# Kernel tuning notes

Hardware: AMD Instinct MI355X
Metric: run time of the kernel (lower is better)

The kernel has to match this reference:

```python
import jax, jax.numpy as jnp
import numpy as np
from jax import lax

IN_CH = 256
NF = 128
B, H, W = 8, 256, 256


def _bn_relu(y, s, b):
    # inference-mode BatchNorm folded into per-channel affine, then ReLU
    return jax.nn.relu(y * s[None, :, None, None] + b[None, :, None, None])


def _upsample_bilinear_ac(x, scale):
    # bilinear upsample, align_corners=True (matches torch nn.Upsample)
    b, c, h, w = x.shape
    Ho, Wo = h * scale, w * scale
    ys = jnp.arange(Ho, dtype=x.dtype) * ((h - 1) / (Ho - 1))
    xs = jnp.arange(Wo, dtype=x.dtype) * ((w - 1) / (Wo - 1))
    y0 = jnp.floor(ys).astype(jnp.int32)
    x0 = jnp.floor(xs).astype(jnp.int32)
    y1 = jnp.minimum(y0 + 1, h - 1)
    x1 = jnp.minimum(x0 + 1, w - 1)
    wy = (ys - y0.astype(x.dtype))[None, None, :, None]
    wx = (xs - x0.astype(x.dtype))[None, None, None, :]
    # interpolate rows then columns
    top = x[:, :, y0, :] * (1 - wy) + x[:, :, y1, :] * wy      # [b,c,Ho,w]
    out = top[:, :, :, x0] * (1 - wx) + top[:, :, :, x1] * wx  # [b,c,Ho,Wo]
    return out


def setup_inputs() -> dict:
    key = jax.random.key(0)
    ks = jax.random.split(key, 6)
    inp = {
        "x": jax.random.normal(ks[0], (B, 64, H, W), dtype=jnp.float32),
        "w1": jax.random.normal(ks[1], (IN_CH, 64, 8, 8), dtype=jnp.float32) * 0.02,
        "bn1_s": jnp.ones((IN_CH,), jnp.float32),
        "bn1_b": jnp.zeros((IN_CH,), jnp.float32),
        "w_fai": jax.random.normal(ks[2], (NF, IN_CH), dtype=jnp.float32) * 0.05,
        "bnf_s": jnp.ones((NF,), jnp.float32),
        "bnf_b": jnp.zeros((NF,), jnp.float32),
        "w_sit": jax.random.normal(ks[3], (NF, IN_CH), dtype=jnp.float32) * 0.05,
        "bns_s": jnp.ones((NF,), jnp.float32),
        "bns_b": jnp.zeros((NF,), jnp.float32),
        "w_gama": jax.random.normal(ks[4], (NF, IN_CH), dtype=jnp.float32) * 0.05,
        "bng_s": jnp.ones((NF,), jnp.float32),
        "bng_b": jnp.zeros((NF,), jnp.float32),
    }
    return inp


def reference(x, w1, bn1_s, bn1_b, w_fai, bnf_s, bnf_b, w_sit, bns_s, bns_b,
              w_gama, bng_s, bng_b):
    # conv1: 8x8 stride-8 conv, BN, ReLU  -> [B, IN_CH, h, w]
    y = lax.conv_general_dilated(x, w1, window_strides=(8, 8), padding="VALID",
                                 dimension_numbers=("NCHW", "OIHW", "NCHW"))
    y = _bn_relu(y, bn1_s, bn1_b)
    b, c, h, w = y.shape
    n = h * w
    # 1x1 conv projections (einsum), BN, ReLU
    fai = _bn_relu(jnp.einsum("bchw,oc->bohw", y, w_fai), bnf_s, bnf_b)
    sit = _bn_relu(jnp.einsum("bchw,oc->bohw", y, w_sit), bns_s, bns_b)
    gama = _bn_relu(jnp.einsum("bchw,oc->bohw", y, w_gama), bng_s, bng_b)
    fai = fai.reshape(b, NF, n)
    sit = sit.reshape(b, NF, n)
    gama = gama.reshape(b, NF, n)
    # non-local attention: sigmoid(fai^T sit) @ gama^T
    sf = jax.nn.sigmoid(jnp.einsum("bcn,bcm->bnm", fai, sit))  # [b, n, n]
    out = jnp.einsum("bnm,bcm->bcn", sf, gama)                  # [b, NF, n]
    out = out.reshape(b, NF, h, w)
    return _upsample_bilinear_ac(out, 8)
```

## Files before the change

kernel.cpp:

```cpp
#include <hip/hip_runtime.h>

typedef __attribute__((ext_vector_type(8))) short short8_t;
typedef __attribute__((ext_vector_type(4))) float float4_t;

__device__ __forceinline__ unsigned short f2bf(float f) {
    unsigned int u = __float_as_uint(f);
    return (unsigned short)((u + 0x7FFFu + ((u >> 16) & 1u)) >> 16);
}
__device__ __forceinline__ unsigned int pkbf(float a, float b) {
    return (unsigned int)f2bf(a) | ((unsigned int)f2bf(b) << 16);
}

__global__ __launch_bounds__(256) void k_wprep(
    const float* __restrict__ w1, unsigned short* __restrict__ w1s)
{
    const int id = blockIdx.x * 256 + threadIdx.x;
    const float4* s = (const float4*)(w1 + id * 8);
    float4 a = s[0], b = s[1];
    int4 o;
    o.x = pkbf(a.x, a.y); o.y = pkbf(a.z, a.w);
    o.z = pkbf(b.x, b.y); o.w = pkbf(b.z, b.w);
    *(int4*)(w1s + id * 8) = o;
}

__global__ __launch_bounds__(256, 2) void k_conv1(
    const float* __restrict__ x, const unsigned short* __restrict__ w1s,
    float* __restrict__ part)
{
    __shared__ unsigned short At[64 * 40];
    __shared__ unsigned short Bt[256 * 40];
    const int tid = threadIdx.x;
    const int mt = blockIdx.x, kc = blockIdx.y;
    const int m0 = mt * 64;
    const int bi = mt >> 4;
    const int oh0 = (mt & 15) * 2;
    const int lane = tid & 63, wid = tid >> 6;
    const int wn = wid;
    const int quad = lane >> 4, r16 = lane & 15;
    const int ow  = tid & 31;
    const int khl = (tid >> 5) & 3;
    const int ohl = tid >> 7;
    const int rowA  = ohl * 32 + ow;
    const int koffA = (khl ^ ((rowA >> 1) & 3)) * 8;
    const int kbase = kc * 1024;
    float4_t acc[4][4] = {};
    float4 ra0, ra1;
    int4 rb[4];

    {
        const int k0 = kbase;
        const int ic = k0 >> 6, kh0 = (k0 >> 3) & 7;
        const int xr = (oh0 + ohl) * 8 + kh0 + khl;
        const float4* s4 = (const float4*)(x + (((bi * 64 + ic) * 256 + xr) * 256 + ow * 8));
        ra0 = s4[0]; ra1 = s4[1];
        #pragma unroll
        for (int l = 0; l < 4; ++l) {
            const int slot = l * 256 + tid;
            const int row = slot >> 2, p = slot & 3;
            rb[l] = *(const int4*)(w1s + row * 4096 + k0 + p * 8);
        }
    }
    for (int it = 0; it < 32; ++it) {
        {
            int4 pa;
            pa.x = pkbf(ra0.x, ra0.y); pa.y = pkbf(ra0.z, ra0.w);
            pa.z = pkbf(ra1.x, ra1.y); pa.w = pkbf(ra1.z, ra1.w);
            *(int4*)&At[rowA * 40 + koffA] = pa;
            #pragma unroll
            for (int l = 0; l < 4; ++l) {
                const int slot = l * 256 + tid;
                const int row = slot >> 2, p = slot & 3;
                *(int4*)&Bt[row * 40 + p * 8] = rb[l];
            }
        }
        __syncthreads();
        if (it + 1 < 32) {
            const int k0 = kbase + (it + 1) * 32;
            const int ic = k0 >> 6, kh0 = (k0 >> 3) & 7;
            const int xr = (oh0 + ohl) * 8 + kh0 + khl;
            const float4* s4 = (const float4*)(x + (((bi * 64 + ic) * 256 + xr) * 256 + ow * 8));
            ra0 = s4[0]; ra1 = s4[1];
            #pragma unroll
            for (int l = 0; l < 4; ++l) {
                const int slot = l * 256 + tid;
                const int row = slot >> 2, p = slot & 3;
                rb[l] = *(const int4*)(w1s + row * 4096 + k0 + p * 8);
            }
        }
        short8_t aF[4], bF[4];
        #pragma unroll
        for (int i = 0; i < 4; ++i) {
            const int R = i * 16 + r16;
            aF[i] = *(const short8_t*)&At[R * 40 + (quad ^ ((r16 >> 1) & 3)) * 8];
        }
        #pragma unroll
        for (int j = 0; j < 4; ++j)
            bF[j] = *(const short8_t*)&Bt[(wn * 64 + j * 16 + r16) * 40 + quad * 8];
        #pragma unroll
        for (int i = 0; i < 4; ++i)
            #pragma unroll
            for (int j = 0; j < 4; ++j)
                acc[i][j] = __builtin_amdgcn_mfma_f32_16x16x32_bf16(aF[i], bF[j], acc[i][j], 0, 0, 0);
        __syncthreads();
    }
    float* pp = part + ((size_t)kc << 21);
    #pragma unroll
    for (int i = 0; i < 4; ++i) {
        const int mg = m0 + i * 16 + quad * 4;
        #pragma unroll
        for (int j = 0; j < 4; ++j) {
            const int ng = wn * 64 + j * 16 + r16;
            #pragma unroll
            for (int r = 0; r < 4; ++r)
                pp[(mg + r) * 256 + ng] = acc[i][j][r];
        }
    }
}

__global__ __launch_bounds__(256, 4) void k_reduce(
    const float* __restrict__ part, const float* __restrict__ s1,
    const float* __restrict__ b1, unsigned short* __restrict__ y)
{
    const int id = blockIdx.x * 256 + threadIdx.x;
    const int c4 = id & 63;
    const float4* p = (const float4*)part + id;
    float4 a = p[0], b = p[524288], c = p[1048576], d = p[1572864];
    float4 s = ((const float4*)s1)[c4], bb = ((const float4*)b1)[c4];
    float vx = fmaxf((a.x + b.x + c.x + d.x) * s.x + bb.x, 0.f);
    float vy = fmaxf((a.y + b.y + c.y + d.y) * s.y + bb.y, 0.f);
    float vz = fmaxf((a.z + b.z + c.z + d.z) * s.z + bb.z, 0.f);
    float vw = fmaxf((a.w + b.w + c.w + d.w) * s.w + bb.w, 0.f);
    int2 o; o.x = pkbf(vx, vy); o.y = pkbf(vz, vw);
    ((int2*)y)[id] = o;
}

__global__ __launch_bounds__(256, 2) void k_proj3(
    const unsigned short* __restrict__ y,
    const float* __restrict__ w_fai, const float* __restrict__ w_sit,
    const float* __restrict__ w_gama,
    const float* __restrict__ fs, const float* __restrict__ fb,
    const float* __restrict__ ss, const float* __restrict__ sb,
    const float* __restrict__ gs, const float* __restrict__ gb,
    unsigned short* __restrict__ P, unsigned short* __restrict__ G)
{
    __shared__ unsigned short At[64 * 40];
    __shared__ unsigned short Bt[64 * 40];
    const int tid = threadIdx.x;
    const int nt = blockIdx.x, mt = blockIdx.y;
    const int m0 = mt * 64;
    const float *W, *S, *Bb;
    if (nt < 2)      { W = w_fai;  S = fs; Bb = fb; }
    else if (nt < 4) { W = w_sit;  S = ss; Bb = sb; }
    else             { W = w_gama; S = gs; Bb = gb; }
    const int roff = (nt * 64) & 127;
    const int lane = tid & 63, wid = tid >> 6;
    const int wm = wid & 1, wn = wid >> 1;
    const int quad = lane >> 4, r16 = lane & 15;
    float4_t acc[2][2] = {};

    for (int k0 = 0; k0 < 256; k0 += 32) {
        {
            const int row = tid >> 2, pp = tid & 3;
            *(int4*)&At[row * 40 + pp * 8] =
                *(const int4*)(y + (m0 + row) * 256 + k0 + pp * 8);
        }
        #pragma unroll
        for (int l = 0; l < 2; ++l) {
            const int slot = l * 256 + tid;
            const int row = slot >> 3, pp = slot & 7;
            float4 v = *(const float4*)(W + (roff + row) * 256 + k0 + pp * 4);
            int2 wv; wv.x = pkbf(v.x, v.y); wv.y = pkbf(v.z, v.w);
            *(int2*)&Bt[row * 40 + pp * 4] = wv;
        }
        __syncthreads();
        short8_t aF[2], bF[2];
        #pragma unroll
        for (int i = 0; i < 2; ++i)
            aF[i] = *(const short8_t*)&At[(wm * 32 + i * 16 + r16) * 40 + quad * 8];
        #pragma unroll
        for (int j = 0; j < 2; ++j)
            bF[j] = *(const short8_t*)&Bt[(wn * 32 + j * 16 + r16) * 40 + quad * 8];
        #pragma unroll
        for (int i = 0; i < 2; ++i)
            #pragma unroll
            for (int j = 0; j < 2; ++j)
                acc[i][j] = __builtin_amdgcn_mfma_f32_16x16x32_bf16(aF[i], bF[j], acc[i][j], 0, 0, 0);
        __syncthreads();
    }
    #pragma unroll
    for (int i = 0; i < 2; ++i) {
        const int mg = m0 + wm * 32 + i * 16 + quad * 4;
        #pragma unroll
        for (int j = 0; j < 2; ++j) {
            const int nl = wn * 32 + j * 16 + r16;
            const float sc = S[roff + nl], bc = Bb[roff + nl];
            if (nt < 4) {
                const int col = nt * 64 + nl;
                #pragma unroll
                for (int r = 0; r < 4; ++r) {
                    float v = fmaxf(acc[i][j][r] * sc + bc, 0.f);
                    P[(mg + r) * 256 + col] = f2bf(v);
                }
            } else {
                const int c = roff + nl;
                #pragma unroll
                for (int r = 0; r < 4; ++r) {
                    float v = fmaxf(acc[i][j][r] * sc + bc, 0.f);
                    const int sp = mg + r;
                    G[((sp >> 10) * 128 + c) * 1024 + (sp & 1023)] = f2bf(v);
                }
            }
        }
    }
}

#define LSTR 152
__global__ __launch_bounds__(256, 2) void k_attn(
    const unsigned short* __restrict__ P, const unsigned short* __restrict__ G,
    float* __restrict__ Opart)
{
    __shared__ unsigned short At[64 * LSTR];
    __shared__ unsigned short Bt[128 * LSTR];
    __shared__ unsigned short Sl[64 * LSTR];
    const int tid = threadIdx.x;
    const int nt = blockIdx.x, zz = blockIdx.y;
    const int b = zz >> 2, kc = zz & 3;
    const int n0 = nt * 64;
    const int base = b * 1024;
    const int lane = tid & 63, wid = tid >> 6;
    const int wm = wid & 1, wn = wid >> 1;
    const int quad = lane >> 4, r16 = lane & 15;
    float4_t acc2[2][4] = {};

    #pragma unroll
    for (int l = 0; l < 4; ++l) {
        const int slot = l * 256 + tid;
        const int row = slot >> 4, p = slot & 15;
        *(int4*)&At[row * LSTR + p * 8] =
            *(const int4*)(P + (base + n0 + row) * 256 + p * 8);
    }
    for (int ms = 0; ms < 2; ++ms) {
        const int m1 = kc * 256 + ms * 128;
        #pragma unroll
        for (int l = 0; l < 8; ++l) {
            const int slot = l * 256 + tid;
            const int row = slot >> 4, p = slot & 15;
            *(int4*)&Bt[row * LSTR + p * 8] =
                *(const int4*)(P + (base + m1 + row) * 256 + 128 + p * 8);
        }
        __syncthreads();
        float4_t acc1[2][4] = {};
        #pragma unroll
        for (int c = 0; c < 4; ++c) {
            short8_t aF[2], bF[4];
            #pragma unroll
            for (int i = 0; i < 2; ++i)
                aF[i] = *(const short8_t*)&At[(wm * 32 + i * 16 + r16) * LSTR + c * 32 + quad * 8];
            #pragma unroll
            for (int j = 0; j < 4; ++j)
                bF[j] = *(const short8_t*)&Bt[(wn * 64 + j * 16 + r16) * LSTR + c * 32 + quad * 8];
            #pragma unroll
            for (int i = 0; i < 2; ++i)
                #pragma unroll
                for (int j = 0; j < 4; ++j)
                    acc1[i][j] = __builtin_amdgcn_mfma_f32_16x16x32_bf16(aF[i], bF[j], acc1[i][j], 0, 0, 0);
        }
        __syncthreads();
        #pragma unroll
        for (int i = 0; i < 2; ++i) {
            const int nl = wm * 32 + i * 16 + quad * 4;
            #pragma unroll
            for (int j = 0; j < 4; ++j) {
                const int ml = wn * 64 + j * 16 + r16;
                #pragma unroll
                for (int r = 0; r < 4; ++r) {
                    const float xv = acc1[i][j][r];
                    const float e = __expf(-xv);
                    const float v = __builtin_amdgcn_rcpf(1.0f + e);
                    Sl[(nl + r) * LSTR + ml] = f2bf(v);
                }
            }
        }
        #pragma unroll
        for (int l = 0; l < 8; ++l) {
            const int slot = l * 256 + tid;
            const int row = slot >> 4, p = slot & 15;
            *(int4*)&Bt[row * LSTR + p * 8] =
                *(const int4*)(G + (b * 128 + row) * 1024 + m1 + p * 8);
        }
        __syncthreads();
        #pragma unroll
        for (int c = 0; c < 4; ++c) {
            short8_t aF[2], bF[4];
            #pragma unroll
            for (int i = 0; i < 2; ++i)
                aF[i] = *(const short8_t*)&Sl[(wm * 32 + i * 16 + r16) * LSTR + c * 32 + quad * 8];
            #pragma unroll
            for (int j = 0; j < 4; ++j)
                bF[j] = *(const short8_t*)&Bt[(wn * 64 + j * 16 + r16) * LSTR + c * 32 + quad * 8];
            #pragma unroll
            for (int i = 0; i < 2; ++i)
                #pragma unroll
                for (int j = 0; j < 4; ++j)
                    acc2[i][j] = __builtin_amdgcn_mfma_f32_16x16x32_bf16(aF[i], bF[j], acc2[i][j], 0, 0, 0);
        }
        __syncthreads();
    }
    float* op = Opart + (size_t)kc * 1048576 + (size_t)b * 131072;
    #pragma unroll
    for (int i = 0; i < 2; ++i) {
        const int nl = n0 + wm * 32 + i * 16 + quad * 4;
        #pragma unroll
        for (int j = 0; j < 4; ++j) {
            const int ch = wn * 64 + j * 16 + r16;
            #pragma unroll
            for (int r = 0; r < 4; ++r)
                op[(nl + r) * 128 + ch] = acc2[i][j][r];
        }
    }
}

__global__ __launch_bounds__(256, 2) void k_up(
    const float* __restrict__ Opart, float* __restrict__ out)
{
    __shared__ float l0[32 * 136];
    __shared__ float l1[32 * 136];
    const int tid = threadIdx.x;
    const int yb = blockIdx.x, b = blockIdx.y;
    const float sc = 31.0f / 255.0f;
    const float fy = yb * sc;
    const int y0 = (int)fy;
    const float wy = fy - (float)y0;
    const int y1 = (y0 + 1 < 32) ? y0 + 1 : 31;
    const float4* r0 = (const float4*)(Opart + (size_t)b * 131072 + y0 * 4096);
    const float4* r1 = (const float4*)(Opart + (size_t)b * 131072 + y1 * 4096);
    #pragma unroll
    for (int j = 0; j < 4; ++j) {
        const int id = j * 256 + tid;
        const int xs = id >> 5, c4 = id & 31;
        float4 a0 = r0[id], a1 = r1[id];
        #pragma unroll
        for (int kc = 1; kc < 4; ++kc) {
            float4 t0 = r0[id + kc * 262144], t1 = r1[id + kc * 262144];
            a0.x += t0.x; a0.y += t0.y; a0.z += t0.z; a0.w += t0.w;
            a1.x += t1.x; a1.y += t1.y; a1.z += t1.z; a1.w += t1.w;
        }
        *(float4*)(l0 + xs * 136 + c4 * 4) = a0;
        *(float4*)(l1 + xs * 136 + c4 * 4) = a1;
    }
    __syncthreads();
    const float fx = tid * sc;
    const int x0 = (int)fx;
    const float wx = fx - (float)x0;
    const int x1 = (x0 + 1 < 32) ? x0 + 1 : 31;
    const float w00 = (1.f - wy) * (1.f - wx), w01 = (1.f - wy) * wx;
    const float w10 = wy * (1.f - wx), w11 = wy * wx;
    const float* a = l0 + x0 * 136;
    const float* bq = l0 + x1 * 136;
    const float* c = l1 + x0 * 136;
    const float* d = l1 + x1 * 136;
    float* op = out + (size_t)b * 8388608 + yb * 256 + tid;
    #pragma unroll 4
    for (int ch = 0; ch < 128; ++ch)
        op[ch * 65536] = w00 * a[ch] + w01 * bq[ch] + w10 * c[ch] + w11 * d[ch];
}

extern "C" void kernel_launch(void* const* d_in, const int* in_sizes, int n_in,
                              void* d_out, int out_size, void* d_ws, size_t ws_size,
                              hipStream_t stream) {
    (void)in_sizes; (void)n_in; (void)out_size; (void)ws_size;
    const float* x      = (const float*)d_in[0];
    const float* w1     = (const float*)d_in[1];
    const float* bn1_s  = (const float*)d_in[2];
    const float* bn1_b  = (const float*)d_in[3];
    const float* w_fai  = (const float*)d_in[4];
    const float* bnf_s  = (const float*)d_in[5];
    const float* bnf_b  = (const float*)d_in[6];
    const float* w_sit  = (const float*)d_in[7];
    const float* bns_s  = (const float*)d_in[8];
    const float* bns_b  = (const float*)d_in[9];
    const float* w_gama = (const float*)d_in[10];
    const float* bng_s  = (const float*)d_in[11];
    const float* bng_b  = (const float*)d_in[12];
    float* out = (float*)d_out;

    char* ws = (char*)d_ws;
    float*          pc    = (float*)ws;
    float*          Opart = (float*)(ws + 16u * 1024 * 1024);
    unsigned short* y     = (unsigned short*)(ws + 32u * 1024 * 1024);
    unsigned short* P     = (unsigned short*)(ws + 36u * 1024 * 1024);
    unsigned short* G     = (unsigned short*)(ws + 40u * 1024 * 1024);
    unsigned short* w1s   = (unsigned short*)(ws + 44u * 1024 * 1024);

    k_wprep <<<dim3(512),      256, 0, stream>>>(w1, w1s);
    k_conv1 <<<dim3(128, 4),   256, 0, stream>>>(x, w1s, pc);
    k_reduce<<<dim3(2048),     256, 0, stream>>>(pc, bn1_s, bn1_b, y);
    k_proj3 <<<dim3(6, 128),   256, 0, stream>>>(y, w_fai, w_sit, w_gama,
                                                 bnf_s, bnf_b, bns_s, bns_b,
                                                 bng_s, bng_b, P, G);
    k_attn  <<<dim3(16, 32),   256, 0, stream>>>(P, G, Opart);
    k_up    <<<dim3(256, 8),   256, 0, stream>>>(Opart, out);
}
```

Baseline: 510.1 us.

## Enlarge conv1 M-tile to 128 with 8 warps and split load roles

```diff
diff --git a/kernel.cpp b/kernel.cpp
--- a/kernel.cpp
+++ b/kernel.cpp
@@ -23,52 +23,58 @@
     *(int4*)(w1s + id * 8) = o;
 }
 
-__global__ __launch_bounds__(256, 2) void k_conv1(
+__global__ __launch_bounds__(512, 2) void k_conv1(
     const float* __restrict__ x, const unsigned short* __restrict__ w1s,
     float* __restrict__ part)
 {
-    __shared__ unsigned short At[64 * 40];
+    __shared__ unsigned short At[128 * 40];
     __shared__ unsigned short Bt[256 * 40];
     const int tid = threadIdx.x;
     const int mt = blockIdx.x, kc = blockIdx.y;
-    const int m0 = mt * 64;
-    const int bi = mt >> 4;
-    const int oh0 = (mt & 15) * 2;
+    const int m0 = mt * 128;
+    const int bi = mt >> 3;
+    const int oh0 = (mt & 7) * 4;
     const int lane = tid & 63, wid = tid >> 6;
-    const int wn = wid;
+    const int wm = wid & 1, wn = wid >> 1;
     const int quad = lane >> 4, r16 = lane & 15;
-    const int ow  = tid & 31;
-    const int khl = (tid >> 5) & 3;
-    const int ohl = tid >> 7;
-    const int rowA  = ohl * 32 + ow;
-    const int koffA = (khl ^ ((rowA >> 1) & 3)) * 8;
+    const bool isA = tid < 256;
+    const int tA = tid & 255;
+    const int rA = tA >> 4, segA = tA & 15;
+    const int ohl = rA >> 2, khl = rA & 3;
+    const int rowA = ohl * 32 + segA * 2;
+    const int koffA = (khl ^ (segA & 3)) * 8;
     const int kbase = kc * 1024;
     float4_t acc[4][4] = {};
-    float4 ra0, ra1;
+    float4 ra[4];
     int4 rb[4];
 
-    {
-        const int k0 = kbase;
-        const int ic = k0 >> 6, kh0 = (k0 >> 3) & 7;
+    if (isA) {
+        const int ic = kbase >> 6, kh0 = (kbase >> 3) & 7;
         const int xr = (oh0 + ohl) * 8 + kh0 + khl;
-        const float4* s4 = (const float4*)(x + (((bi * 64 + ic) * 256 + xr) * 256 + ow * 8));
-        ra0 = s4[0]; ra1 = s4[1];
+        const float4* s4 = (const float4*)(x + (((bi * 64 + ic) * 256 + xr) * 256 + segA * 16));
+        ra[0] = s4[0]; ra[1] = s4[1]; ra[2] = s4[2]; ra[3] = s4[3];
+    } else {
         #pragma unroll
         for (int l = 0; l < 4; ++l) {
-            const int slot = l * 256 + tid;
+            const int slot = l * 256 + tA;
             const int row = slot >> 2, p = slot & 3;
-            rb[l] = *(const int4*)(w1s + row * 4096 + k0 + p * 8);
-        }
-    }
+            rb[l] = *(const int4*)(w1s + row * 4096 + kbase + p * 8);
+        }
+    }
+
     for (int it = 0; it < 32; ++it) {
-        {
-            int4 pa;
-            pa.x = pkbf(ra0.x, ra0.y); pa.y = pkbf(ra0.z, ra0.w);
-            pa.z = pkbf(ra1.x, ra1.y); pa.w = pkbf(ra1.z, ra1.w);
-            *(int4*)&At[rowA * 40 + koffA] = pa;
+        if (isA) {
+            int4 p0, p1;
+            p0.x = pkbf(ra[0].x, ra[0].y); p0.y = pkbf(ra[0].z, ra[0].w);
+            p0.z = pkbf(ra[1].x, ra[1].y); p0.w = pkbf(ra[1].z, ra[1].w);
+            p1.x = pkbf(ra[2].x, ra[2].y); p1.y = pkbf(ra[2].z, ra[2].w);
+            p1.z = pkbf(ra[3].x, ra[3].y); p1.w = pkbf(ra[3].z, ra[3].w);
+            *(int4*)&At[rowA * 40 + koffA] = p0;
+            *(int4*)&At[(rowA + 1) * 40 + koffA] = p1;
+        } else {
             #pragma unroll
             for (int l = 0; l < 4; ++l) {
-                const int slot = l * 256 + tid;
+                const int slot = l * 256 + tA;
                 const int row = slot >> 2, p = slot & 3;
                 *(int4*)&Bt[row * 40 + p * 8] = rb[l];
             }
@@ -76,21 +82,24 @@
         __syncthreads();
         if (it + 1 < 32) {
             const int k0 = kbase + (it + 1) * 32;
-            const int ic = k0 >> 6, kh0 = (k0 >> 3) & 7;
-            const int xr = (oh0 + ohl) * 8 + kh0 + khl;
-            const float4* s4 = (const float4*)(x + (((bi * 64 + ic) * 256 + xr) * 256 + ow * 8));
-            ra0 = s4[0]; ra1 = s4[1];
-            #pragma unroll
-            for (int l = 0; l < 4; ++l) {
-                const int slot = l * 256 + tid;
-                const int row = slot >> 2, p = slot & 3;
-                rb[l] = *(const int4*)(w1s + row * 4096 + k0 + p * 8);
+            if (isA) {
+                const int ic = k0 >> 6, kh0 = (k0 >> 3) & 7;
+                const int xr = (oh0 + ohl) * 8 + kh0 + khl;
+                const float4* s4 = (const float4*)(x + (((bi * 64 + ic) * 256 + xr) * 256 + segA * 16));
+                ra[0] = s4[0]; ra[1] = s4[1]; ra[2] = s4[2]; ra[3] = s4[3];
+            } else {
+                #pragma unroll
+                for (int l = 0; l < 4; ++l) {
+                    const int slot = l * 256 + tA;
+                    const int row = slot >> 2, p = slot & 3;
+                    rb[l] = *(const int4*)(w1s + row * 4096 + k0 + p * 8);
+                }
             }
         }
         short8_t aF[4], bF[4];
         #pragma unroll
         for (int i = 0; i < 4; ++i) {
-            const int R = i * 16 + r16;
+            const int R = wm * 64 + i * 16 + r16;
             aF[i] = *(const short8_t*)&At[R * 40 + (quad ^ ((r16 >> 1) & 3)) * 8];
         }
         #pragma unroll
@@ -106,7 +115,7 @@
     float* pp = part + ((size_t)kc << 21);
     #pragma unroll
     for (int i = 0; i < 4; ++i) {
-        const int mg = m0 + i * 16 + quad * 4;
+        const int mg = m0 + wm * 64 + i * 16 + quad * 4;
         #pragma unroll
         for (int j = 0; j < 4; ++j) {
             const int ng = wn * 64 + j * 16 + r16;
@@ -393,7 +402,7 @@
     unsigned short* w1s   = (unsigned short*)(ws + 44u * 1024 * 1024);
 
     k_wprep <<<dim3(512),      256, 0, stream>>>(w1, w1s);
-    k_conv1 <<<dim3(128, 4),   256, 0, stream>>>(x, w1s, pc);
+    k_conv1 <<<dim3(64, 4),    512, 0, stream>>>(x, w1s, pc);
     k_reduce<<<dim3(2048),     256, 0, stream>>>(pc, bn1_s, bn1_b, y);
     k_proj3 <<<dim3(6, 128),   256, 0, stream>>>(y, w_fai, w_sit, w_gama,
                                                  bnf_s, bnf_b, bns_s, bns_b,
```

New measurement: 472.8 us, median of 2. 7.3% less time.
